# Optimization experiments

Measured on AMD Instinct MI355X. Metric: run time of the kernel, lower is better.

## Reference

```python
import jax, jax.numpy as jnp
import numpy as np

B, L, D, A = 64, 512, 512, 512  # batch, seq_len, word_embed_size, alignment_size


def setup_inputs() -> dict:
    key = jax.random.key(0)
    k1, k2, k3 = jax.random.split(key, 3)
    premises = jax.random.normal(k1, (B, L, D), dtype=jnp.float32)
    hypotheses = jax.random.normal(k2, (B, L, D), dtype=jnp.float32)
    W_F = jax.random.uniform(k3, (D, A), dtype=jnp.float32, minval=-1.0, maxval=1.0)
    return {"premises": premises, "hypotheses": hypotheses, "W_F": W_F}


def reference(premises, hypotheses, W_F):
    # tanh-projected cross attention (decomposable-attention align step)
    F_p = jnp.tanh(jnp.einsum('bpd,da->bpa', premises, W_F))    # [B, Lp, A]
    F_h = jnp.tanh(jnp.einsum('bhd,da->bha', hypotheses, W_F))  # [B, Lh, A]
    eijs = jnp.einsum('bpa,bha->bph', F_p, F_h)                 # [B, Lp, Lh] (unscaled)
    attn = jax.nn.softmax(eijs, axis=-1)                        # softmax over hypothesis axis
    betas = jnp.einsum('bph,bhd->bpd', attn, hypotheses)        # [B, Lp, D]
    alphas = jnp.einsum('bph,bpd->bhd', attn, premises)         # [B, Lh, D] (transpose(attn) @ P)
    return betas, alphas
```

## Files before the change

### kernel.cpp

```cpp
#include <hip/hip_runtime.h>
#include <hip/hip_fp16.h>


#define NB 64
#define NL 512
#define ND 512
#define BATCH_ELEMS (512 * 512)
#define TOT_ELEMS   ((size_t)NB * NL * ND)

typedef _Float16 h8 __attribute__((ext_vector_type(8)));
typedef float f4 __attribute__((ext_vector_type(4)));

__device__ __forceinline__ int swz(int row, int chunk) {
    return (row << 5) + ((chunk ^ ((row >> 1) & 3)) << 3);
}

__device__ __forceinline__ float fast_tanh(float x) {
    float e = __expf(2.0f * x);
    return 1.0f - 2.0f / (e + 1.0f);
}

__global__ __launch_bounds__(256) void proj_tanh_kernel(
    const float* __restrict__ P, const float* __restrict__ H,
    const float* __restrict__ W, _Float16* __restrict__ Fout)
{
    __shared__ __align__(16) _Float16 AsH[128 * 32], AsL[128 * 32];
    __shared__ __align__(16) _Float16 BsH[128 * 32], BsL[128 * 32];

    const int z = blockIdx.z;
    const float* X = z ? H : P;
    _Float16* F = Fout + (size_t)z * TOT_ELEMS;
    const int r0 = blockIdx.y * 128;
    const int n0 = blockIdx.x * 128;

    const int t = threadIdx.x;
    const int lane = t & 63, w = t >> 6;
    const int q = lane >> 4, c = lane & 15;
    const int wm = w >> 1, wn = w & 1;

    f4 acc[4][4] = {};

    const int ar = t >> 1, akq = (t & 1) << 4;
    const int bk = t >> 3, bn0 = (t & 7) << 4;

    for (int k0 = 0; k0 < 512; k0 += 32) {
        {
            const float* ap = X + (size_t)(r0 + ar) * 512 + k0 + akq;
            float av[16];
            *(float4*)&av[0]  = ((const float4*)ap)[0];
            *(float4*)&av[4]  = ((const float4*)ap)[1];
            *(float4*)&av[8]  = ((const float4*)ap)[2];
            *(float4*)&av[12] = ((const float4*)ap)[3];
            const int cbase = akq >> 3;
#pragma unroll
            for (int jj = 0; jj < 2; ++jj) {
                h8 hv, lv;
#pragma unroll
                for (int i = 0; i < 8; ++i) {
                    float x = av[jj * 8 + i];
                    _Float16 hx = (_Float16)x;
                    hv[i] = hx;
                    lv[i] = (_Float16)(x - (float)hx);
                }
                *(h8*)&AsH[swz(ar, cbase + jj)] = hv;
                *(h8*)&AsL[swz(ar, cbase + jj)] = lv;
            }
        }
        {
            const float* bp = W + (size_t)(k0 + bk) * 512 + n0 + bn0;
            float bv[16];
            *(float4*)&bv[0]  = ((const float4*)bp)[0];
            *(float4*)&bv[4]  = ((const float4*)bp)[1];
            *(float4*)&bv[8]  = ((const float4*)bp)[2];
            *(float4*)&bv[12] = ((const float4*)bp)[3];
#pragma unroll
            for (int j = 0; j < 16; ++j) {
                int n = bn0 + j;
                int off = swz(n, bk >> 3) + (bk & 7);
                _Float16 hx = (_Float16)bv[j];
                BsH[off] = hx;
                BsL[off] = (_Float16)(bv[j] - (float)hx);
            }
        }
        __syncthreads();

        h8 aH[4], aL[4], bH[4], bL[4];
#pragma unroll
        for (int mi = 0; mi < 4; ++mi) {
            int row = wm * 64 + mi * 16 + c;
            aH[mi] = *(const h8*)&AsH[swz(row, q)];
            aL[mi] = *(const h8*)&AsL[swz(row, q)];
        }
#pragma unroll
        for (int ni = 0; ni < 4; ++ni) {
            int col = wn * 64 + ni * 16 + c;
            bH[ni] = *(const h8*)&BsH[swz(col, q)];
            bL[ni] = *(const h8*)&BsL[swz(col, q)];
        }
#pragma unroll
        for (int mi = 0; mi < 4; ++mi)
#pragma unroll
            for (int ni = 0; ni < 4; ++ni) {
                acc[mi][ni] = __builtin_amdgcn_mfma_f32_16x16x32_f16(aH[mi], bH[ni], acc[mi][ni], 0, 0, 0);
                acc[mi][ni] = __builtin_amdgcn_mfma_f32_16x16x32_f16(aH[mi], bL[ni], acc[mi][ni], 0, 0, 0);
                acc[mi][ni] = __builtin_amdgcn_mfma_f32_16x16x32_f16(aL[mi], bH[ni], acc[mi][ni], 0, 0, 0);
            }
        __syncthreads();
    }

#pragma unroll
    for (int mi = 0; mi < 4; ++mi)
#pragma unroll
        for (int ni = 0; ni < 4; ++ni) {
            int col = n0 + wn * 64 + ni * 16 + c;
            int rowb = r0 + wm * 64 + mi * 16 + q * 4;
#pragma unroll
            for (int r = 0; r < 4; ++r)
                F[(size_t)(rowb + r) * 512 + col] = (_Float16)fast_tanh(acc[mi][ni][r]);
        }
}

__global__ __launch_bounds__(256) void score_softmax_kernel(
    const _Float16* __restrict__ Fbase, _Float16* __restrict__ attn)
{
    __shared__ __align__(16) _Float16 As[64 * 32];
    __shared__ __align__(16) _Float16 Bs[512 * 32];
    __shared__ float redM[4 * 64], redS[4 * 64];

    const _Float16* Fp = Fbase;
    const _Float16* Fh = Fbase + TOT_ELEMS;
    const int b = blockIdx.y;
    const int p0 = blockIdx.x * 64;
    const size_t fb = (size_t)b * BATCH_ELEMS;

    const int t = threadIdx.x, lane = t & 63, w = t >> 6;
    const int q = lane >> 4, c = lane & 15;

    f4 acc[4][8] = {};

    for (int k0 = 0; k0 < 512; k0 += 32) {
        {
            int row = t >> 2, ch = t & 3;
            *(h8*)&As[swz(row, ch)] =
                *(const h8*)(Fp + fb + (size_t)(p0 + row) * 512 + k0 + ch * 8);
        }
        {
#pragma unroll
            for (int rr = 0; rr < 2; ++rr) {
                int row = t * 2 + rr;
#pragma unroll
                for (int ch = 0; ch < 4; ++ch)
                    *(h8*)&Bs[swz(row, ch)] =
                        *(const h8*)(Fh + fb + (size_t)row * 512 + k0 + ch * 8);
            }
        }
        __syncthreads();

        h8 a[4], bb[8];
#pragma unroll
        for (int mt = 0; mt < 4; ++mt) a[mt] = *(const h8*)&As[swz(mt * 16 + c, q)];
#pragma unroll
        for (int nt = 0; nt < 8; ++nt) bb[nt] = *(const h8*)&Bs[swz(w * 128 + nt * 16 + c, q)];
#pragma unroll
        for (int mt = 0; mt < 4; ++mt)
#pragma unroll
            for (int nt = 0; nt < 8; ++nt)
                acc[mt][nt] = __builtin_amdgcn_mfma_f32_16x16x32_f16(a[mt], bb[nt], acc[mt][nt], 0, 0, 0);
        __syncthreads();
    }

    float rmax[4][4];
#pragma unroll
    for (int mt = 0; mt < 4; ++mt)
#pragma unroll
        for (int r = 0; r < 4; ++r) {
            float m = acc[mt][0][r];
#pragma unroll
            for (int nt = 1; nt < 8; ++nt) m = fmaxf(m, acc[mt][nt][r]);
            rmax[mt][r] = m;
        }
#pragma unroll
    for (int s = 1; s < 16; s <<= 1)
#pragma unroll
        for (int mt = 0; mt < 4; ++mt)
#pragma unroll
            for (int r = 0; r < 4; ++r)
                rmax[mt][r] = fmaxf(rmax[mt][r], __shfl_xor(rmax[mt][r], s, 64));
    if (c == 0)
#pragma unroll
        for (int mt = 0; mt < 4; ++mt)
#pragma unroll
            for (int r = 0; r < 4; ++r)
                redM[w * 64 + mt * 16 + q * 4 + r] = rmax[mt][r];
    __syncthreads();

    float gmax[4][4];
#pragma unroll
    for (int mt = 0; mt < 4; ++mt)
#pragma unroll
        for (int r = 0; r < 4; ++r) {
            int row = mt * 16 + q * 4 + r;
            float m = redM[row];
#pragma unroll
            for (int w4 = 1; w4 < 4; ++w4) m = fmaxf(m, redM[w4 * 64 + row]);
            gmax[mt][r] = m;
        }

    float rsum[4][4] = {};
#pragma unroll
    for (int mt = 0; mt < 4; ++mt)
#pragma unroll
        for (int nt = 0; nt < 8; ++nt)
#pragma unroll
            for (int r = 0; r < 4; ++r) {
                float e = __expf(acc[mt][nt][r] - gmax[mt][r]);
                acc[mt][nt][r] = e;
                rsum[mt][r] += e;
            }
#pragma unroll
    for (int s = 1; s < 16; s <<= 1)
#pragma unroll
        for (int mt = 0; mt < 4; ++mt)
#pragma unroll
            for (int r = 0; r < 4; ++r)
                rsum[mt][r] += __shfl_xor(rsum[mt][r], s, 64);
    if (c == 0)
#pragma unroll
        for (int mt = 0; mt < 4; ++mt)
#pragma unroll
            for (int r = 0; r < 4; ++r)
                redS[w * 64 + mt * 16 + q * 4 + r] = rsum[mt][r];
    __syncthreads();

    float inv[4][4];
#pragma unroll
    for (int mt = 0; mt < 4; ++mt)
#pragma unroll
        for (int r = 0; r < 4; ++r) {
            int row = mt * 16 + q * 4 + r;
            float s = redS[row] + redS[64 + row] + redS[128 + row] + redS[192 + row];
            inv[mt][r] = 1.0f / s;
        }

#pragma unroll
    for (int mt = 0; mt < 4; ++mt)
#pragma unroll
        for (int nt = 0; nt < 8; ++nt) {
            int col = w * 128 + nt * 16 + c;
#pragma unroll
            for (int r = 0; r < 4; ++r) {
                int row = p0 + mt * 16 + q * 4 + r;
                attn[fb + (size_t)row * 512 + col] = (_Float16)(acc[mt][nt][r] * inv[mt][r]);
            }
        }
}

template <bool TRANS_A>
__global__ __launch_bounds__(256) void out_gemm_kernel(
    const _Float16* __restrict__ Amat, const float* __restrict__ Bmat,
    float* __restrict__ Cout)
{
    __shared__ __align__(16) _Float16 As[128 * 32];
    __shared__ __align__(16) _Float16 Bs[128 * 32];

    const int b = blockIdx.z;
    const int bn = blockIdx.x * 128, bm = blockIdx.y * 128;
    const size_t base = (size_t)b * BATCH_ELEMS;

    const int t = threadIdx.x, lane = t & 63, w = t >> 6;
    const int q = lane >> 4, c = lane & 15;
    const int wm = w >> 1, wn = w & 1;

    f4 acc[4][4] = {};

    for (int k0 = 0; k0 < 512; k0 += 32) {
        if (!TRANS_A) {
            int row = t >> 1, cp = (t & 1) * 2;
            const _Float16* ap = Amat + base + (size_t)(bm + row) * 512 + k0 + cp * 8;
            *(h8*)&As[swz(row, cp)]     = ((const h8*)ap)[0];
            *(h8*)&As[swz(row, cp + 1)] = ((const h8*)ap)[1];
        } else {
            int kk = t >> 3, m0 = (t & 7) * 16;
            const _Float16* ap = Amat + base + (size_t)(k0 + kk) * 512 + bm + m0;
            h8 x0 = ((const h8*)ap)[0];
            h8 x1 = ((const h8*)ap)[1];
#pragma unroll
            for (int j = 0; j < 8; ++j) {
                As[swz(m0 + j, kk >> 3) + (kk & 7)]     = x0[j];
                As[swz(m0 + 8 + j, kk >> 3) + (kk & 7)] = x1[j];
            }
        }
        {
            int kk = t >> 3, n0l = (t & 7) * 16;
            const float* bp = Bmat + base + (size_t)(k0 + kk) * 512 + bn + n0l;
            float bv[16];
            *(float4*)&bv[0]  = ((const float4*)bp)[0];
            *(float4*)&bv[4]  = ((const float4*)bp)[1];
            *(float4*)&bv[8]  = ((const float4*)bp)[2];
            *(float4*)&bv[12] = ((const float4*)bp)[3];
#pragma unroll
            for (int j = 0; j < 16; ++j)
                Bs[swz(n0l + j, kk >> 3) + (kk & 7)] = (_Float16)bv[j];
        }
        __syncthreads();

        h8 a[4], bb[4];
#pragma unroll
        for (int mi = 0; mi < 4; ++mi) a[mi] = *(const h8*)&As[swz(wm * 64 + mi * 16 + c, q)];
#pragma unroll
        for (int ni = 0; ni < 4; ++ni) bb[ni] = *(const h8*)&Bs[swz(wn * 64 + ni * 16 + c, q)];
#pragma unroll
        for (int mi = 0; mi < 4; ++mi)
#pragma unroll
            for (int ni = 0; ni < 4; ++ni)
                acc[mi][ni] = __builtin_amdgcn_mfma_f32_16x16x32_f16(a[mi], bb[ni], acc[mi][ni], 0, 0, 0);
        __syncthreads();
    }

#pragma unroll
    for (int mi = 0; mi < 4; ++mi)
#pragma unroll
        for (int ni = 0; ni < 4; ++ni) {
            int col = bn + wn * 64 + ni * 16 + c;
            int rowb = bm + wm * 64 + mi * 16 + q * 4;
#pragma unroll
            for (int r = 0; r < 4; ++r)
                Cout[base + (size_t)(rowb + r) * 512 + col] = acc[mi][ni][r];
        }
}

extern "C" void kernel_launch(void* const* d_in, const int* in_sizes, int n_in,
                              void* d_out, int out_size, void* d_ws, size_t ws_size,
                              hipStream_t stream) {
    const float* P = (const float*)d_in[0];
    const float* H = (const float*)d_in[1];
    const float* W = (const float*)d_in[2];
    float* out = (float*)d_out;

    _Float16* F    = (_Float16*)d_ws;
    _Float16* attn = F + 2 * TOT_ELEMS;

    proj_tanh_kernel<<<dim3(4, 256, 2), 256, 0, stream>>>(P, H, W, F);
    score_softmax_kernel<<<dim3(8, NB), 256, 0, stream>>>(F, attn);
    out_gemm_kernel<false><<<dim3(4, 4, NB), 256, 0, stream>>>(attn, H, out);
    out_gemm_kernel<true><<<dim3(4, 4, NB), 256, 0, stream>>>(attn, P, out + TOT_ELEMS);
}
```

Baseline: 587.0 us.

## Pre-transpose W, H and P to fp16 so GEMM B-tiles load vectorized

New measurement: 499.7 us. 1.17x faster.

```diff
diff --git a/kernel.cpp b/kernel.cpp
--- a/kernel.cpp
+++ b/kernel.cpp
@@ -12,7 +12,7 @@
 typedef float f4 __attribute__((ext_vector_type(4)));
 
 __device__ __forceinline__ int swz(int row, int chunk) {
-    return (row << 5) + ((chunk ^ ((row >> 1) & 3)) << 3);
+    return (row << 5) + ((chunk ^ (((row >> 1) ^ (row >> 4)) & 3)) << 3);
 }
 
 __device__ __forceinline__ float fast_tanh(float x) {
@@ -20,9 +20,48 @@
     return 1.0f - 2.0f / (e + 1.0f);
 }
 
+template <bool WITH_LO>
+__global__ __launch_bounds__(256) void transpose_f16_kernel(
+    const float* __restrict__ src, _Float16* __restrict__ dstH,
+    _Float16* __restrict__ dstL)
+{
+    __shared__ float tile[64 * 68];
+    const size_t base = (size_t)blockIdx.z * BATCH_ELEMS;
+    const int r0 = blockIdx.y * 64, c0 = blockIdx.x * 64;
+    const int t = threadIdx.x;
+    {
+        int r = t >> 2, cq = (t & 3) * 16;
+        const float* sp = src + base + (size_t)(r0 + r) * 512 + c0 + cq;
+        *(float4*)&tile[r * 68 + cq]      = ((const float4*)sp)[0];
+        *(float4*)&tile[r * 68 + cq + 4]  = ((const float4*)sp)[1];
+        *(float4*)&tile[r * 68 + cq + 8]  = ((const float4*)sp)[2];
+        *(float4*)&tile[r * 68 + cq + 12] = ((const float4*)sp)[3];
+    }
+    __syncthreads();
+    {
+        int c = t >> 2, rq = (t & 3) * 16;
+        _Float16 hv[16], lv[16];
+#pragma unroll
+        for (int j = 0; j < 16; ++j) {
+            float v = tile[(rq + j) * 68 + c];
+            hv[j] = (_Float16)v;
+            if (WITH_LO) lv[j] = (_Float16)(v - (float)hv[j]);
+        }
+        _Float16* dp = dstH + base + (size_t)(c0 + c) * 512 + r0 + rq;
+        *(h8*)dp = *(h8*)&hv[0];
+        *(h8*)(dp + 8) = *(h8*)&hv[8];
+        if (WITH_LO) {
+            _Float16* dl = dstL + base + (size_t)(c0 + c) * 512 + r0 + rq;
+            *(h8*)dl = *(h8*)&lv[0];
+            *(h8*)(dl + 8) = *(h8*)&lv[8];
+        }
+    }
+}
+
 __global__ __launch_bounds__(256) void proj_tanh_kernel(
     const float* __restrict__ P, const float* __restrict__ H,
-    const float* __restrict__ W, _Float16* __restrict__ Fout)
+    const _Float16* __restrict__ WTH, const _Float16* __restrict__ WTL,
+    _Float16* __restrict__ Fout)
 {
     __shared__ __align__(16) _Float16 AsH[128 * 32], AsL[128 * 32];
     __shared__ __align__(16) _Float16 BsH[128 * 32], BsL[128 * 32];
@@ -30,8 +69,8 @@
     const int z = blockIdx.z;
     const float* X = z ? H : P;
     _Float16* F = Fout + (size_t)z * TOT_ELEMS;
-    const int r0 = blockIdx.y * 128;
-    const int n0 = blockIdx.x * 128;
+    const int r0 = blockIdx.x * 128;
+    const int n0 = blockIdx.y * 128;
 
     const int t = threadIdx.x;
     const int lane = t & 63, w = t >> 6;
@@ -41,7 +80,7 @@
     f4 acc[4][4] = {};
 
     const int ar = t >> 1, akq = (t & 1) << 4;
-    const int bk = t >> 3, bn0 = (t & 7) << 4;
+    const int br = t >> 1, bcp = (t & 1) << 1;
 
     for (int k0 = 0; k0 < 512; k0 += 32) {
         {
@@ -67,20 +106,12 @@
             }
         }
         {
-            const float* bp = W + (size_t)(k0 + bk) * 512 + n0 + bn0;
-            float bv[16];
-            *(float4*)&bv[0]  = ((const float4*)bp)[0];
-            *(float4*)&bv[4]  = ((const float4*)bp)[1];
-            *(float4*)&bv[8]  = ((const float4*)bp)[2];
-            *(float4*)&bv[12] = ((const float4*)bp)[3];
-#pragma unroll
-            for (int j = 0; j < 16; ++j) {
-                int n = bn0 + j;
-                int off = swz(n, bk >> 3) + (bk & 7);
-                _Float16 hx = (_Float16)bv[j];
-                BsH[off] = hx;
-                BsL[off] = (_Float16)(bv[j] - (float)hx);
-            }
+            const _Float16* bh = WTH + (size_t)(n0 + br) * 512 + k0 + bcp * 8;
+            const _Float16* bl = WTL + (size_t)(n0 + br) * 512 + k0 + bcp * 8;
+            *(h8*)&BsH[swz(br, bcp)]     = ((const h8*)bh)[0];
+            *(h8*)&BsH[swz(br, bcp + 1)] = ((const h8*)bh)[1];
+            *(h8*)&BsL[swz(br, bcp)]     = ((const h8*)bl)[0];
+            *(h8*)&BsL[swz(br, bcp + 1)] = ((const h8*)bl)[1];
         }
         __syncthreads();
 
@@ -257,7 +288,7 @@
 
 template <bool TRANS_A>
 __global__ __launch_bounds__(256) void out_gemm_kernel(
-    const _Float16* __restrict__ Amat, const float* __restrict__ Bmat,
+    const _Float16* __restrict__ Amat, const _Float16* __restrict__ BT,
     float* __restrict__ Cout)
 {
     __shared__ __align__(16) _Float16 As[128 * 32];
@@ -291,16 +322,10 @@
             }
         }
         {
-            int kk = t >> 3, n0l = (t & 7) * 16;
-            const float* bp = Bmat + base + (size_t)(k0 + kk) * 512 + bn + n0l;
-            float bv[16];
-            *(float4*)&bv[0]  = ((const float4*)bp)[0];
-            *(float4*)&bv[4]  = ((const float4*)bp)[1];
-            *(float4*)&bv[8]  = ((const float4*)bp)[2];
-            *(float4*)&bv[12] = ((const float4*)bp)[3];
-#pragma unroll
-            for (int j = 0; j < 16; ++j)
-                Bs[swz(n0l + j, kk >> 3) + (kk & 7)] = (_Float16)bv[j];
+            int row = t >> 1, cp = (t & 1) * 2;
+            const _Float16* bp = BT + base + (size_t)(bn + row) * 512 + k0 + cp * 8;
+            *(h8*)&Bs[swz(row, cp)]     = ((const h8*)bp)[0];
+            *(h8*)&Bs[swz(row, cp + 1)] = ((const h8*)bp)[1];
         }
         __syncthreads();
 
@@ -337,11 +362,19 @@
     const float* W = (const float*)d_in[2];
     float* out = (float*)d_out;
 
-    _Float16* F    = (_Float16*)d_ws;
-    _Float16* attn = F + 2 * TOT_ELEMS;
-
-    proj_tanh_kernel<<<dim3(4, 256, 2), 256, 0, stream>>>(P, H, W, F);
+    _Float16* ws16 = (_Float16*)d_ws;
+    _Float16* F    = ws16;
+    _Float16* PT   = ws16;
+    _Float16* HT   = ws16 + TOT_ELEMS;
+    _Float16* attn = ws16 + 2 * TOT_ELEMS;
+    _Float16* WTH  = attn;
+    _Float16* WTL  = attn + BATCH_ELEMS;
+
+    transpose_f16_kernel<true><<<dim3(8, 8, 1), 256, 0, stream>>>(W, WTH, WTL);
+    proj_tanh_kernel<<<dim3(256, 4, 2), 256, 0, stream>>>(P, H, WTH, WTL, F);
     score_softmax_kernel<<<dim3(8, NB), 256, 0, stream>>>(F, attn);
-    out_gemm_kernel<false><<<dim3(4, 4, NB), 256, 0, stream>>>(attn, H, out);
-    out_gemm_kernel<true><<<dim3(4, 4, NB), 256, 0, stream>>>(attn, P, out + TOT_ELEMS);
-}
+    transpose_f16_kernel<false><<<dim3(8, 8, NB), 256, 0, stream>>>(H, HT, nullptr);
+    transpose_f16_kernel<false><<<dim3(8, 8, NB), 256, 0, stream>>>(P, PT, nullptr);
+    out_gemm_kernel<false><<<dim3(4, 4, NB), 256, 0, stream>>>(attn, HT, out);
+    out_gemm_kernel<true><<<dim3(4, 4, NB), 256, 0, stream>>>(attn, PT, out + TOT_ELEMS);
+}
```
